# Optimization experiments

Hardware: AMD Instinct MI355X
Metric: run time of the kernel (lower is better)

The kernel has to match this reference:

```python
import jax, jax.numpy as jnp
import numpy as np
import math

DIM = 1024
THETA = 10000.0


def rope_cos_sin(seq_len, dim, dtype=jnp.float32):
    # freqs over pairs: 1/theta^(2i/dim), angles = t * freq
    inv = 1.0 / (THETA ** (jnp.arange(0, dim, 2, dtype=jnp.float32) / dim))  # [dim/2]
    t = jnp.arange(seq_len, dtype=jnp.float32)
    ang = jnp.outer(t, inv)  # [S, dim/2]
    return jnp.cos(ang).astype(dtype), jnp.sin(ang).astype(dtype)


def apply_rotary(x, cos, sin):
    # x: [B, S, D]; treat consecutive pairs as complex (xr + i*xi)
    B, S, D = x.shape
    xr = x[..., 0::2]  # [B, S, D/2]
    xi = x[..., 1::2]
    or_ = xr * cos - xi * sin
    oi_ = xr * sin + xi * cos
    # interleave back: (..., D/2, 2) -> (..., D)
    return jnp.stack([or_, oi_], axis=-1).reshape(B, S, D)


def setup_inputs() -> dict:
    key = jax.random.key(0)
    ks = jax.random.split(key, 5)
    B, S, D = 4, 2048, DIM
    x = jax.random.normal(ks[0], (B, S, D), dtype=jnp.float32)
    s = 1.0 / math.sqrt(D)
    wq = jax.random.normal(ks[1], (D, D), dtype=jnp.float32) * s
    wk = jax.random.normal(ks[2], (D, D), dtype=jnp.float32) * s
    wv = jax.random.normal(ks[3], (D, D), dtype=jnp.float32) * s
    wo = jax.random.normal(ks[4], (D, D), dtype=jnp.float32) * s
    return {"x": x, "wq": wq, "wk": wk, "wv": wv, "wo": wo}


def reference(x, wq, wk, wv, wo):
    B, S, D = x.shape
    xq = jnp.einsum('bsd,ed->bse', x, wq)  # Linear: x @ W^T
    xk = jnp.einsum('bsd,ed->bse', x, wk)
    xv = jnp.einsum('bsd,ed->bse', x, wv)
    cos, sin = rope_cos_sin(S, D, x.dtype)
    xq = apply_rotary(xq, cos, sin)
    xk = apply_rotary(xk, cos, sin)
    scores = jnp.einsum('bqd,bkd->bqk', xq, xk) / jnp.sqrt(jnp.asarray(D, x.dtype))
    attn = jax.nn.softmax(scores, axis=-1)  # no causal mask in original
    out = jnp.einsum('bqk,bkd->bqd', attn, xv)
    return jnp.einsum('bsd,ed->bse', out, wo)
```

## Files before the change

### kernel.cpp

```cpp
#include <hip/hip_runtime.h>
#include <math.h>

typedef __attribute__((ext_vector_type(8))) short short8;
typedef __attribute__((ext_vector_type(4))) float f32x4;
typedef unsigned short u16;

__device__ __forceinline__ float b2f(u16 u) {
    union { unsigned u; float f; } c; c.u = ((unsigned)u) << 16; return c.f;
}
__device__ __forceinline__ u16 f2b(float f) {
    unsigned u = __float_as_uint(f);
    u += 0x7fffu + ((u >> 16) & 1u);
    return (u16)(u >> 16);
}

__device__ __forceinline__ void gl_lds16(const u16* g, u16* l) {
    __builtin_amdgcn_global_load_lds(
        (const __attribute__((address_space(1))) void*)g,
        (__attribute__((address_space(3))) void*)l,
        16, 0, 0);
}

__global__ __launch_bounds__(256) void cvt_f32_bf16(const float* __restrict__ src,
                                                    u16* __restrict__ dst, int n) {
    const int i = (blockIdx.x * 256 + threadIdx.x) * 8;
    if (i >= n) return;
    const float4 a = *(const float4*)&src[i];
    const float4 b = *(const float4*)&src[i + 4];
    short8 o;
    o[0] = (short)f2b(a.x); o[1] = (short)f2b(a.y);
    o[2] = (short)f2b(a.z); o[3] = (short)f2b(a.w);
    o[4] = (short)f2b(b.x); o[5] = (short)f2b(b.y);
    o[6] = (short)f2b(b.z); o[7] = (short)f2b(b.w);
    *(short8*)&dst[i] = o;
}

__global__ __launch_bounds__(256) void cvt_weights(
    const float* __restrict__ w0, const float* __restrict__ w1,
    const float* __restrict__ w2, const float* __restrict__ w3,
    u16* __restrict__ dst) {
    const int z = blockIdx.z;
    const float* src = (z == 0) ? w0 : (z == 1) ? w1 : (z == 2) ? w2 : w3;
    const int i = (blockIdx.x * 256 + threadIdx.x) * 8;
    const float4 a = *(const float4*)&src[i];
    const float4 b = *(const float4*)&src[i + 4];
    short8 o;
    o[0] = (short)f2b(a.x); o[1] = (short)f2b(a.y);
    o[2] = (short)f2b(a.z); o[3] = (short)f2b(a.w);
    o[4] = (short)f2b(b.x); o[5] = (short)f2b(b.y);
    o[6] = (short)f2b(b.z); o[7] = (short)f2b(b.w);
    *(short8*)&dst[(long)z * 1024 * 1024 + i] = o;
}

template<typename OT>
__device__ __forceinline__ void gemm_body(
    const u16* __restrict__ A, const u16* __restrict__ W, OT* __restrict__ C,
    int lda, int ldw, int ldc, int K, float scale)
{
    __shared__ u16 lsA[2][128 * 32];
    __shared__ u16 lsB[2][128 * 32];

    const int m0 = blockIdx.y * 128;
    const int n0 = blockIdx.x * 128;
    const int t = threadIdx.x;
    const int lane = t & 63;
    const int wave = t >> 6;
    const int wm = (wave & 1) * 64;
    const int wn = (wave >> 1) * 64;

    const int sr = t >> 2;
    const int scol = ((t & 3) ^ ((t >> 3) & 3)) * 8;

    const u16* pa0 = A + (long)(m0 + sr) * lda + scol;
    const u16* pa1 = pa0 + (long)64 * lda;
    const u16* pw0 = W + (long)(n0 + sr) * ldw + scol;
    const u16* pw1 = pw0 + (long)64 * ldw;

    f32x4 acc[4][4];
#pragma unroll
    for (int i = 0; i < 4; ++i)
#pragma unroll
        for (int j = 0; j < 4; ++j)
            acc[i][j] = (f32x4){0.f, 0.f, 0.f, 0.f};

    const int fr = lane & 15;
    const int fq = lane >> 4;
    const int swz = (fq ^ ((fr >> 1) & 3)) * 8;
    const int aoff = (wm + fr) * 32 + swz;
    const int boff = (wn + fr) * 32 + swz;

    gl_lds16(pa0, &lsA[0][t * 8]);        pa0 += 32;
    gl_lds16(pa1, &lsA[0][2048 + t * 8]); pa1 += 32;
    gl_lds16(pw0, &lsB[0][t * 8]);        pw0 += 32;
    gl_lds16(pw1, &lsB[0][2048 + t * 8]); pw1 += 32;

    const int nsteps = K >> 5;
    int par = 0;
    for (int s = 0; s < nsteps; ++s) {
        __syncthreads();
        if (s + 1 < nsteps) {
            const int np = par ^ 1;
            gl_lds16(pa0, &lsA[np][t * 8]);        pa0 += 32;
            gl_lds16(pa1, &lsA[np][2048 + t * 8]); pa1 += 32;
            gl_lds16(pw0, &lsB[np][t * 8]);        pw0 += 32;
            gl_lds16(pw1, &lsB[np][2048 + t * 8]); pw1 += 32;
        }

        short8 af[4], bf[4];
#pragma unroll
        for (int i = 0; i < 4; ++i)
            af[i] = *(const short8*)&lsA[par][aoff + i * 512];
#pragma unroll
        for (int j = 0; j < 4; ++j)
            bf[j] = *(const short8*)&lsB[par][boff + j * 512];
#pragma unroll
        for (int i = 0; i < 4; ++i)
#pragma unroll
            for (int j = 0; j < 4; ++j)
                acc[i][j] = __builtin_amdgcn_mfma_f32_16x16x32_bf16(af[i], bf[j], acc[i][j], 0, 0, 0);
        par ^= 1;
    }

#pragma unroll
    for (int i = 0; i < 4; ++i) {
#pragma unroll
        for (int j = 0; j < 4; ++j) {
            const int row0 = m0 + wm + i * 16 + fq * 4;
            const int col = n0 + wn + j * 16 + fr;
#pragma unroll
            for (int r = 0; r < 4; ++r) {
                const int row = row0 + r;
                const float val = acc[i][j][r] * scale;
                if (sizeof(OT) == 2) {
                    ((u16*)C)[(long)row * ldc + col] = f2b(val);
                } else {
                    ((float*)C)[(long)row * ldc + col] = val;
                }
            }
        }
    }
}

template<typename OT>
__global__ __launch_bounds__(256) void gemm_bt(
    const u16* __restrict__ A, const u16* __restrict__ W, OT* __restrict__ C,
    int lda, int ldw, int ldc, int K,
    long sA, long sW, long sC, float scale)
{
    const int bz = blockIdx.z;
    gemm_body<OT>(A + (long)bz * sA, W + (long)bz * sW, C + (long)bz * sC,
                  lda, ldw, ldc, K, scale);
}

__global__ __launch_bounds__(256) void gemm_dual(
    const u16* __restrict__ A0, const u16* __restrict__ W0, u16* __restrict__ C0,
    int lda0, int ldw0, int ldc0, long sA0, long sW0, long sC0, float scale0,
    const u16* __restrict__ A1, const u16* __restrict__ W1, u16* __restrict__ C1,
    int lda1, int ldw1, int ldc1, long sA1, long sW1, long sC1, float scale1)
{
    const int z = blockIdx.z;
    if (z < 4) {
        gemm_body<u16>(A0 + (long)z * sA0, W0 + (long)z * sW0, C0 + (long)z * sC0,
                       lda0, ldw0, ldc0, 1024, scale0);
    } else {
        if (blockIdx.y >= 8) return;
        const int b = z - 4;
        gemm_body<u16>(A1 + (long)b * sA1, W1 + (long)b * sW1, C1 + (long)b * sC1,
                       lda1, ldw1, ldc1, 1024, scale1);
    }
}

__global__ __launch_bounds__(256) void rope_kernel(u16* q, u16* k) {
    const int row = blockIdx.x;
    const int pos = row & 2047;
    u16* p = (blockIdx.y ? k : q) + (long)row * 1024;
#pragma unroll
    for (int it = 0; it < 2; ++it) {
        const int i = threadIdx.x + it * 256;
        const float e = (float)i * (1.0f / 512.0f);
        const float inv = powf(10000.0f, -e);
        const float ang = (float)pos * inv;
        float s, c;
        sincosf(ang, &s, &c);
        const float xr = b2f(p[2 * i]);
        const float xi = b2f(p[2 * i + 1]);
        p[2 * i]     = f2b(xr * c - xi * s);
        p[2 * i + 1] = f2b(xr * s + xi * c);
    }
}

__global__ __launch_bounds__(256) void softmax_kernel(const u16* __restrict__ S, u16* __restrict__ P) {
    const long row = blockIdx.x;
    const u16* src = S + row * 2048;
    u16* dst = P + row * 2048;
    const int t = threadIdx.x;
    const int lane = t & 63;
    const int wave = t >> 6;
    __shared__ float red[4];

    float v[8];
    const short8 raw = *(const short8*)&src[t * 8];
#pragma unroll
    for (int i = 0; i < 8; ++i) v[i] = b2f((u16)raw[i]);

    float m = v[0];
#pragma unroll
    for (int i = 1; i < 8; ++i) m = fmaxf(m, v[i]);
    for (int o = 32; o > 0; o >>= 1) m = fmaxf(m, __shfl_xor(m, o, 64));
    if (lane == 0) red[wave] = m;
    __syncthreads();
    m = fmaxf(fmaxf(red[0], red[1]), fmaxf(red[2], red[3]));
    __syncthreads();

    float sum = 0.f;
#pragma unroll
    for (int i = 0; i < 8; ++i) { v[i] = expf(v[i] - m); sum += v[i]; }
    for (int o = 32; o > 0; o >>= 1) sum += __shfl_xor(sum, o, 64);
    if (lane == 0) red[wave] = sum;
    __syncthreads();
    sum = red[0] + red[1] + red[2] + red[3];
    const float is = 1.0f / sum;

    short8 outv;
#pragma unroll
    for (int i = 0; i < 8; ++i) outv[i] = (short)f2b(v[i] * is);
    *(short8*)&dst[t * 8] = outv;
}

extern "C" void kernel_launch(void* const* d_in, const int* in_sizes, int n_in,
                              void* d_out, int out_size, void* d_ws, size_t ws_size,
                              hipStream_t stream)
{
    (void)in_sizes; (void)n_in; (void)out_size; (void)ws_size;
    const float* x  = (const float*)d_in[0];
    const float* wq = (const float*)d_in[1];
    const float* wk = (const float*)d_in[2];
    const float* wv = (const float*)d_in[3];
    const float* wo = (const float*)d_in[4];
    float* out = (float*)d_out;

    const long M1 = 1024 * 1024;
    u16* ws  = (u16*)d_ws;
    u16* xb  = ws;
    u16* wqb = xb + 8 * M1;
    u16* wob = wqb + 3 * M1;
    u16* q   = wqb + 4 * M1;
    u16* kk  = q + 8 * M1;
    u16* v   = kk + 8 * M1;
    u16* sc  = v + 8 * M1;
    u16* UT  = xb;

    const dim3 blk(256);

    cvt_f32_bf16<<<dim3(4096), blk, 0, stream>>>(x, xb, 8 * 1024 * 1024);
    cvt_weights<<<dim3(512, 1, 4), blk, 0, stream>>>(wq, wk, wv, wo, wqb);

    gemm_bt<u16><<<dim3(8, 64, 3), blk, 0, stream>>>(xb, wqb, q,
        1024, 1024, 1024, 1024, 0, M1, 8 * M1, 1.0f);

    rope_kernel<<<dim3(8192, 2), blk, 0, stream>>>(q, kk);

    gemm_dual<<<dim3(16, 16, 8), blk, 0, stream>>>(
        q, kk, sc, 1024, 1024, 2048, 2 * M1, 2 * M1, 4 * M1, 0.03125f,
        wob, v, UT, 1024, 1024, 2048, 0, 2 * M1, 2 * M1, 1.0f);

    softmax_kernel<<<dim3(8192), blk, 0, stream>>>(sc, sc);

    gemm_bt<float><<<dim3(8, 16, 4), blk, 0, stream>>>(sc, UT, out,
        2048, 2048, 1024, 2048, 4 * M1, 2 * M1, 2 * M1, 1.0f);
}
```

Baseline: 332.2 us.

## Use 256x256-tile 512-thread MFMA GEMM for QKV and score/UT projections

Adds a new GEMM body with 256x256 output tiles, 8 waves per block, a 64-wide K step split into two 32-wide halves, and double-buffered direct global-to-LDS loads. Each wave now computes a 128x64 sub-tile, and MFMA issue is raised in priority with s_setprio. The QKV projection and the fused scores/Wo·V launch switch to this kernel, aiming for more data reuse per LDS load and fewer blocks. The trade-offs: the grids shrink to 384 blocks, which risks poor wave quantization on the CUs, the 128KB LDS footprint allows only one block per CU, and the XOR swizzle used before is dropped, which may cause LDS bank conflicts.

Result: no change. 326.3 us (-1.8%).

```diff
diff --git a/kernel.cpp b/kernel.cpp
--- a/kernel.cpp
+++ b/kernel.cpp
@@ -19,6 +19,12 @@
         (const __attribute__((address_space(1))) void*)g,
         (__attribute__((address_space(3))) void*)l,
         16, 0, 0);
+}
+
+__device__ __forceinline__ void wgbar() {
+    asm volatile("" ::: "memory");
+    __builtin_amdgcn_s_barrier();
+    asm volatile("" ::: "memory");
 }
 
 __global__ __launch_bounds__(256) void cvt_f32_bf16(const float* __restrict__ src,
@@ -53,6 +59,136 @@
 }
 
 template<typename OT>
+__device__ __forceinline__ void gemm256_body(
+    const u16* __restrict__ A, const u16* __restrict__ W, OT* __restrict__ C,
+    int lda, int ldw, int ldc, int K, float scale)
+{
+    __shared__ u16 lsA[2][2][8192];
+    __shared__ u16 lsB[2][2][8192];
+
+    const int m0 = blockIdx.y * 256;
+    const int n0 = blockIdx.x * 256;
+    const int t = threadIdx.x;
+    const int lane = t & 63;
+    const int w = t >> 6;
+    const int wm = (w & 1) * 128;
+    const int wn = (w >> 1) * 64;
+    const int fr = lane & 15;
+    const int fq = lane >> 4;
+
+    const int srow = t >> 2;
+    const int scol = (t & 3) * 8;
+    const u16* pA0 = A + (long)(m0 + srow) * lda + scol;
+    const u16* pA1 = A + (long)(m0 + 128 + srow) * lda + scol;
+    const u16* pW0 = W + (long)(n0 + srow) * ldw + scol;
+    const u16* pW1 = W + (long)(n0 + 128 + srow) * ldw + scol;
+    const int tld = t * 8;
+
+    f32x4 acc[8][4];
+#pragma unroll
+    for (int i = 0; i < 8; ++i)
+#pragma unroll
+        for (int j = 0; j < 4; ++j)
+            acc[i][j] = (f32x4){0.f, 0.f, 0.f, 0.f};
+
+    const int aoff = (wm + fr) * 32 + fq * 8;
+    const int boff = (wn + fr) * 32 + fq * 8;
+
+#define STAGE256(buf, h, ko) do { \
+    gl_lds16(pA0 + (ko), &lsA[buf][h][tld]); \
+    gl_lds16(pA1 + (ko), &lsA[buf][h][4096 + tld]); \
+    gl_lds16(pW0 + (ko), &lsB[buf][h][tld]); \
+    gl_lds16(pW1 + (ko), &lsB[buf][h][4096 + tld]); \
+} while (0)
+
+    const int nt = K >> 6;
+    STAGE256(0, 0, 0);
+    STAGE256(0, 1, 32);
+    asm volatile("s_waitcnt vmcnt(4)" ::: "memory");
+    wgbar();
+
+    for (int tt = 0; tt < nt; ++tt) {
+        const int p = tt & 1;
+        const int kn = (tt + 1) << 6;
+#pragma unroll
+        for (int h = 0; h < 2; ++h) {
+            short8 af[8], bfr[4];
+#pragma unroll
+            for (int m = 0; m < 8; ++m)
+                af[m] = *(const short8*)&lsA[p][h][aoff + m * 512];
+#pragma unroll
+            for (int n = 0; n < 4; ++n)
+                bfr[n] = *(const short8*)&lsB[p][h][boff + n * 512];
+            if (tt + 1 < nt) {
+                STAGE256(p ^ 1, h, kn + h * 32);
+                asm volatile("s_waitcnt vmcnt(4)" ::: "memory");
+            } else {
+                asm volatile("s_waitcnt vmcnt(0)" ::: "memory");
+            }
+            wgbar();
+            __builtin_amdgcn_s_setprio(1);
+#pragma unroll
+            for (int m = 0; m < 8; ++m)
+#pragma unroll
+                for (int n = 0; n < 4; ++n)
+                    acc[m][n] = __builtin_amdgcn_mfma_f32_16x16x32_bf16(
+                        af[m], bfr[n], acc[m][n], 0, 0, 0);
+            __builtin_amdgcn_s_setprio(0);
+        }
+    }
+#undef STAGE256
+
+#pragma unroll
+    for (int m = 0; m < 8; ++m) {
+        const int row0 = m0 + wm + m * 16 + fq * 4;
+#pragma unroll
+        for (int n = 0; n < 4; ++n) {
+            const int col = n0 + wn + n * 16 + fr;
+#pragma unroll
+            for (int r = 0; r < 4; ++r) {
+                const float val = acc[m][n][r] * scale;
+                if (sizeof(OT) == 2) {
+                    ((u16*)C)[(long)(row0 + r) * ldc + col] = f2b(val);
+                } else {
+                    ((float*)C)[(long)(row0 + r) * ldc + col] = val;
+                }
+            }
+        }
+    }
+}
+
+template<typename OT>
+__global__ __launch_bounds__(512, 2) void gemm256_bt(
+    const u16* __restrict__ A, const u16* __restrict__ W, OT* __restrict__ C,
+    int lda, int ldw, int ldc, int K,
+    long sA, long sW, long sC, float scale)
+{
+    const int z = blockIdx.z;
+    gemm256_body<OT>(A + (long)z * sA, W + (long)z * sW, C + (long)z * sC,
+                     lda, ldw, ldc, K, scale);
+}
+
+__global__ __launch_bounds__(512, 2) void gemm256_dual(
+    const u16* __restrict__ A0, const u16* __restrict__ W0, u16* __restrict__ C0,
+    int lda0, int ldw0, int ldc0, long sA0, long sW0, long sC0, float scale0,
+    const u16* __restrict__ A1, const u16* __restrict__ W1, u16* __restrict__ C1,
+    int lda1, int ldw1, int ldc1, long sA1, long sW1, long sC1, float scale1)
+{
+    const int z = blockIdx.z;
+    const u16 *A, *W; u16 *C; int lda, ldw, ldc; float scl;
+    if (z < 4) {
+        A = A0 + (long)z * sA0; W = W0 + (long)z * sW0; C = C0 + (long)z * sC0;
+        lda = lda0; ldw = ldw0; ldc = ldc0; scl = scale0;
+    } else {
+        if (blockIdx.y >= 4) return;
+        const int b = z - 4;
+        A = A1 + (long)b * sA1; W = W1 + (long)b * sW1; C = C1 + (long)b * sC1;
+        lda = lda1; ldw = ldw1; ldc = ldc1; scl = scale1;
+    }
+    gemm256_body<u16>(A, W, C, lda, ldw, ldc, 1024, scl);
+}
+
+template<typename OT>
 __device__ __forceinline__ void gemm_body(
     const u16* __restrict__ A, const u16* __restrict__ W, OT* __restrict__ C,
     int lda, int ldw, int ldc, int K, float scale)
@@ -152,24 +288,6 @@
                   lda, ldw, ldc, K, scale);
 }
 
-__global__ __launch_bounds__(256) void gemm_dual(
-    const u16* __restrict__ A0, const u16* __restrict__ W0, u16* __restrict__ C0,
-    int lda0, int ldw0, int ldc0, long sA0, long sW0, long sC0, float scale0,
-    const u16* __restrict__ A1, const u16* __restrict__ W1, u16* __restrict__ C1,
-    int lda1, int ldw1, int ldc1, long sA1, long sW1, long sC1, float scale1)
-{
-    const int z = blockIdx.z;
-    if (z < 4) {
-        gemm_body<u16>(A0 + (long)z * sA0, W0 + (long)z * sW0, C0 + (long)z * sC0,
-                       lda0, ldw0, ldc0, 1024, scale0);
-    } else {
-        if (blockIdx.y >= 8) return;
-        const int b = z - 4;
-        gemm_body<u16>(A1 + (long)b * sA1, W1 + (long)b * sW1, C1 + (long)b * sC1,
-                       lda1, ldw1, ldc1, 1024, scale1);
-    }
-}
-
 __global__ __launch_bounds__(256) void rope_kernel(u16* q, u16* k) {
     const int row = blockIdx.x;
     const int pos = row & 2047;
@@ -251,16 +369,17 @@
     u16* UT  = xb;
 
     const dim3 blk(256);
+    const dim3 blk5(512);
 
     cvt_f32_bf16<<<dim3(4096), blk, 0, stream>>>(x, xb, 8 * 1024 * 1024);
     cvt_weights<<<dim3(512, 1, 4), blk, 0, stream>>>(wq, wk, wv, wo, wqb);
 
-    gemm_bt<u16><<<dim3(8, 64, 3), blk, 0, stream>>>(xb, wqb, q,
+    gemm256_bt<u16><<<dim3(4, 32, 3), blk5, 0, stream>>>(xb, wqb, q,
         1024, 1024, 1024, 1024, 0, M1, 8 * M1, 1.0f);
 
     rope_kernel<<<dim3(8192, 2), blk, 0, stream>>>(q, kk);
 
-    gemm_dual<<<dim3(16, 16, 8), blk, 0, stream>>>(
+    gemm256_dual<<<dim3(8, 8, 8), blk5, 0, stream>>>(
         q, kk, sc, 1024, 1024, 2048, 2 * M1, 2 * M1, 4 * M1, 0.03125f,
         wob, v, UT, 1024, 1024, 2048, 0, 2 * M1, 2 * M1, 1.0f);
 
```

## Fuse RoPE into QKV GEMM epilogue and merge conversion kernels

Applied to the files above, without the earlier changes.

Applies the rotary embedding inside the QKV projection GEMM epilogue for the Q and K slices, so the standalone rope kernel and its read-modify-write pass over Q and K disappear. The partner element of each pair comes from a cross-lane shuffle of the fp32 accumulator. The two fp32-to-bf16 conversion kernels are also merged into one launch. The epilogue now does per-element sincosf, which adds ALU work and register pressure to the GEMM. Rotation in fp32 before rounding slightly changes numerics.

Result: slower. 788.6 us (+137.4%).

```diff
diff --git a/kernel.cpp b/kernel.cpp
--- a/kernel.cpp
+++ b/kernel.cpp
@@ -21,41 +21,38 @@
         16, 0, 0);
 }
 
-__global__ __launch_bounds__(256) void cvt_f32_bf16(const float* __restrict__ src,
-                                                    u16* __restrict__ dst, int n) {
-    const int i = (blockIdx.x * 256 + threadIdx.x) * 8;
-    if (i >= n) return;
+__global__ __launch_bounds__(256) void cvt_all(
+    const float* __restrict__ x,
+    const float* __restrict__ w0, const float* __restrict__ w1,
+    const float* __restrict__ w2, const float* __restrict__ w3,
+    u16* __restrict__ xb, u16* __restrict__ wb)
+{
+    const int b = blockIdx.x;
+    const float* src; u16* dst; int i;
+    if (b < 4096) {
+        i = (b * 256 + threadIdx.x) * 8;
+        src = x; dst = xb;
+    } else {
+        const int j = b - 4096;
+        const int z = j >> 9;
+        src = (z == 0) ? w0 : (z == 1) ? w1 : (z == 2) ? w2 : w3;
+        i = ((j & 511) * 256 + threadIdx.x) * 8;
+        dst = wb + (long)z * 1024 * 1024;
+    }
     const float4 a = *(const float4*)&src[i];
-    const float4 b = *(const float4*)&src[i + 4];
+    const float4 c = *(const float4*)&src[i + 4];
     short8 o;
     o[0] = (short)f2b(a.x); o[1] = (short)f2b(a.y);
     o[2] = (short)f2b(a.z); o[3] = (short)f2b(a.w);
-    o[4] = (short)f2b(b.x); o[5] = (short)f2b(b.y);
-    o[6] = (short)f2b(b.z); o[7] = (short)f2b(b.w);
+    o[4] = (short)f2b(c.x); o[5] = (short)f2b(c.y);
+    o[6] = (short)f2b(c.z); o[7] = (short)f2b(c.w);
     *(short8*)&dst[i] = o;
-}
-
-__global__ __launch_bounds__(256) void cvt_weights(
-    const float* __restrict__ w0, const float* __restrict__ w1,
-    const float* __restrict__ w2, const float* __restrict__ w3,
-    u16* __restrict__ dst) {
-    const int z = blockIdx.z;
-    const float* src = (z == 0) ? w0 : (z == 1) ? w1 : (z == 2) ? w2 : w3;
-    const int i = (blockIdx.x * 256 + threadIdx.x) * 8;
-    const float4 a = *(const float4*)&src[i];
-    const float4 b = *(const float4*)&src[i + 4];
-    short8 o;
-    o[0] = (short)f2b(a.x); o[1] = (short)f2b(a.y);
-    o[2] = (short)f2b(a.z); o[3] = (short)f2b(a.w);
-    o[4] = (short)f2b(b.x); o[5] = (short)f2b(b.y);
-    o[6] = (short)f2b(b.z); o[7] = (short)f2b(b.w);
-    *(short8*)&dst[(long)z * 1024 * 1024 + i] = o;
 }
 
 template<typename OT>
 __device__ __forceinline__ void gemm_body(
     const u16* __restrict__ A, const u16* __restrict__ W, OT* __restrict__ C,
-    int lda, int ldw, int ldc, int K, float scale)
+    int lda, int ldw, int ldc, int K, float scale, bool doRope)
 {
     __shared__ u16 lsA[2][128 * 32];
     __shared__ u16 lsB[2][128 * 32];
@@ -121,27 +118,55 @@
         par ^= 1;
     }
 
-#pragma unroll
-    for (int i = 0; i < 4; ++i) {
+    if (sizeof(OT) == 2 && doRope) {
+        float invf[4];
 #pragma unroll
         for (int j = 0; j < 4; ++j) {
+            const int col = n0 + wn + j * 16 + fr;
+            invf[j] = powf(10000.0f, -(float)(col >> 1) * (1.0f / 512.0f));
+        }
+#pragma unroll
+        for (int i = 0; i < 4; ++i) {
             const int row0 = m0 + wm + i * 16 + fq * 4;
-            const int col = n0 + wn + j * 16 + fr;
-#pragma unroll
-            for (int r = 0; r < 4; ++r) {
-                const int row = row0 + r;
-                const float val = acc[i][j][r] * scale;
-                if (sizeof(OT) == 2) {
-                    ((u16*)C)[(long)row * ldc + col] = f2b(val);
-                } else {
-                    ((float*)C)[(long)row * ldc + col] = val;
+#pragma unroll
+            for (int j = 0; j < 4; ++j) {
+                const int col = n0 + wn + j * 16 + fr;
+                const float sign = (col & 1) ? 1.0f : -1.0f;
+#pragma unroll
+                for (int r = 0; r < 4; ++r) {
+                    const int row = row0 + r;
+                    const float self = acc[i][j][r];
+                    const float other = __shfl_xor(self, 1, 64);
+                    const float ang = (float)(row & 2047) * invf[j];
+                    float sn, cs;
+                    sincosf(ang, &sn, &cs);
+                    ((u16*)C)[(long)row * ldc + col] = f2b(self * cs + sign * other * sn);
                 }
             }
         }
-    }
-}
-
-template<typename OT>
+    } else {
+#pragma unroll
+        for (int i = 0; i < 4; ++i) {
+#pragma unroll
+            for (int j = 0; j < 4; ++j) {
+                const int row0 = m0 + wm + i * 16 + fq * 4;
+                const int col = n0 + wn + j * 16 + fr;
+#pragma unroll
+                for (int r = 0; r < 4; ++r) {
+                    const int row = row0 + r;
+                    const float val = acc[i][j][r] * scale;
+                    if (sizeof(OT) == 2) {
+                        ((u16*)C)[(long)row * ldc + col] = f2b(val);
+                    } else {
+                        ((float*)C)[(long)row * ldc + col] = val;
+                    }
+                }
+            }
+        }
+    }
+}
+
+template<typename OT, bool ROPE>
 __global__ __launch_bounds__(256) void gemm_bt(
     const u16* __restrict__ A, const u16* __restrict__ W, OT* __restrict__ C,
     int lda, int ldw, int ldc, int K,
@@ -149,7 +174,7 @@
 {
     const int bz = blockIdx.z;
     gemm_body<OT>(A + (long)bz * sA, W + (long)bz * sW, C + (long)bz * sC,
-                  lda, ldw, ldc, K, scale);
+                  lda, ldw, ldc, K, scale, ROPE && (bz < 2));
 }
 
 __global__ __launch_bounds__(256) void gemm_dual(
@@ -161,31 +186,12 @@
     const int z = blockIdx.z;
     if (z < 4) {
         gemm_body<u16>(A0 + (long)z * sA0, W0 + (long)z * sW0, C0 + (long)z * sC0,
-                       lda0, ldw0, ldc0, 1024, scale0);
+                       lda0, ldw0, ldc0, 1024, scale0, false);
     } else {
         if (blockIdx.y >= 8) return;
         const int b = z - 4;
         gemm_body<u16>(A1 + (long)b * sA1, W1 + (long)b * sW1, C1 + (long)b * sC1,
-                       lda1, ldw1, ldc1, 1024, scale1);
-    }
-}
-
-__global__ __launch_bounds__(256) void rope_kernel(u16* q, u16* k) {
-    const int row = blockIdx.x;
-    const int pos = row & 2047;
-    u16* p = (blockIdx.y ? k : q) + (long)row * 1024;
-#pragma unroll
-    for (int it = 0; it < 2; ++it) {
-        const int i = threadIdx.x + it * 256;
-        const float e = (float)i * (1.0f / 512.0f);
-        const float inv = powf(10000.0f, -e);
-        const float ang = (float)pos * inv;
-        float s, c;
-        sincosf(ang, &s, &c);
-        const float xr = b2f(p[2 * i]);
-        const float xi = b2f(p[2 * i + 1]);
-        p[2 * i]     = f2b(xr * c - xi * s);
-        p[2 * i + 1] = f2b(xr * s + xi * c);
+                       lda1, ldw1, ldc1, 1024, scale1, false);
     }
 }
 
@@ -252,13 +258,10 @@
 
     const dim3 blk(256);
 
-    cvt_f32_bf16<<<dim3(4096), blk, 0, stream>>>(x, xb, 8 * 1024 * 1024);
-    cvt_weights<<<dim3(512, 1, 4), blk, 0, stream>>>(wq, wk, wv, wo, wqb);
-
-    gemm_bt<u16><<<dim3(8, 64, 3), blk, 0, stream>>>(xb, wqb, q,
+    cvt_all<<<dim3(6144), blk, 0, stream>>>(x, wq, wk, wv, wo, xb, wqb);
+
+    gemm_bt<u16, true><<<dim3(8, 64, 3), blk, 0, stream>>>(xb, wqb, q,
         1024, 1024, 1024, 1024, 0, M1, 8 * M1, 1.0f);
-
-    rope_kernel<<<dim3(8192, 2), blk, 0, stream>>>(q, kk);
 
     gemm_dual<<<dim3(16, 16, 8), blk, 0, stream>>>(
         q, kk, sc, 1024, 1024, 2048, 2 * M1, 2 * M1, 4 * M1, 0.03125f,
@@ -266,6 +269,6 @@
 
     softmax_kernel<<<dim3(8192), blk, 0, stream>>>(sc, sc);
 
-    gemm_bt<float><<<dim3(8, 16, 4), blk, 0, stream>>>(sc, UT, out,
+    gemm_bt<float, false><<<dim3(8, 16, 4), blk, 0, stream>>>(sc, UT, out,
         2048, 2048, 1024, 2048, 4 * M1, 2 * M1, 2 * M1, 1.0f);
 }
```
